# Kernel tuning notes

Measured on AMD Instinct MI355X. Metric: run time of the kernel, lower is better.

The kernel has to match this reference:

```python
import jax, jax.numpy as jnp
import numpy as np
import math

B, S, D, H = 16, 1024, 1024, 16
HD = D // H                      # 64 head dim
MLP_H = int(int(D * 4.0) * 2 / 3)  # 2730 SwiGLU hidden
EPS = 1e-6


def _rmsnorm(h, w):
    # fp32 RMSNorm over last dim
    v = jnp.mean(h * h, axis=-1, keepdims=True)
    return w * (h * jax.lax.rsqrt(v + EPS))


def _rope(x):
    # x: [B, H, S, HD]; standard rotary, half-split convention
    hd = x.shape[-1]
    pos = jnp.arange(x.shape[-2], dtype=jnp.float32)
    inv = 1.0 / (10000.0 ** (jnp.arange(0, hd, 2, dtype=jnp.float32) / hd))
    fr = pos[:, None] * inv[None, :]          # [S, HD/2]
    cos, sin = jnp.cos(fr), jnp.sin(fr)
    x1, x2 = jnp.split(x, 2, axis=-1)
    return jnp.concatenate([x1 * cos - x2 * sin, x1 * sin + x2 * cos], axis=-1)


def setup_inputs() -> dict:
    key = jax.random.key(0)
    ks = jax.random.split(key, 16)
    sc = 0.02
    return {
        "x": jax.random.normal(ks[0], (B, S, D), jnp.float32),
        "c": jax.random.normal(ks[1], (B, D), jnp.float32),
        "w_qkv": jax.random.normal(ks[2], (D, 3 * D), jnp.float32) * sc,
        "b_qkv": jnp.zeros((3 * D,), jnp.float32),
        "w_proj": jax.random.normal(ks[3], (D, D), jnp.float32) * sc,
        "b_proj": jnp.zeros((D,), jnp.float32),
        "w12": jax.random.normal(ks[4], (D, 2 * MLP_H), jnp.float32) * sc,
        "b12": jnp.zeros((2 * MLP_H,), jnp.float32),
        "w3": jax.random.normal(ks[5], (MLP_H, D), jnp.float32) * sc,
        "b3": jnp.zeros((D,), jnp.float32),
        "w_ada": jax.random.normal(ks[6], (D, 6 * D), jnp.float32) * sc,
        "b_ada": jnp.zeros((6 * D,), jnp.float32),
        "norm1_w": jnp.ones((D,), jnp.float32),
        "norm2_w": jnp.ones((D,), jnp.float32),
        "qn_w": jnp.ones((HD,), jnp.float32),
        "kn_w": jnp.ones((HD,), jnp.float32),
    }


def _forward(x, c, w_qkv, b_qkv, w_proj, b_proj, w12, b12, w3, b3,
             w_ada, b_ada, norm1_w, norm2_w, qn_w, kn_w):
    # adaLN modulation params
    ada = jax.nn.silu(c) @ w_ada + b_ada               # [B, 6D]
    sh_a, sc_a, g_a, sh_m, sc_m, g_m = jnp.split(ada, 6, axis=-1)

    def modulate(h, shift, scale):
        return h * (1.0 + scale[:, None, :]) + shift[:, None, :]

    # --- attention branch ---
    h = modulate(_rmsnorm(x, norm1_w), sh_a, sc_a)     # [B, S, D]
    qkv = (h @ w_qkv + b_qkv).reshape(B, S, 3, H, HD)
    qkv = jnp.transpose(qkv, (2, 0, 3, 1, 4))          # [3, B, H, S, HD]
    q, k, v = qkv[0], qkv[1], qkv[2]
    q = _rope(_rmsnorm(q, qn_w))
    k = _rope(_rmsnorm(k, kn_w))
    scores = jnp.einsum('bhqd,bhkd->bhqk', q, k) / math.sqrt(HD)
    attn = jax.nn.softmax(scores, axis=-1)
    o = jnp.einsum('bhqk,bhkd->bhqd', attn, v)         # [B, H, S, HD]
    o = jnp.transpose(o, (0, 2, 1, 3)).reshape(B, S, D)
    o = o @ w_proj + b_proj
    x = x + g_a[:, None, :] * o

    # --- SwiGLU MLP branch ---
    h = modulate(_rmsnorm(x, norm2_w), sh_m, sc_m)
    x12 = h @ w12 + b12
    x1, x2 = jnp.split(x12, 2, axis=-1)
    mlp = (jax.nn.silu(x1) * x2) @ w3 + b3
    return x + g_m[:, None, :] * mlp


def reference(x, c, w_qkv, b_qkv, w_proj, b_proj, w12, b12, w3, b3,
              w_ada, b_ada, norm1_w, norm2_w, qn_w, kn_w):
    return _forward(x, c, w_qkv, b_qkv, w_proj, b_proj, w12, b12, w3, b3,
                    w_ada, b_ada, norm1_w, norm2_w, qn_w, kn_w)
```

## Files before the change

kernel.cpp:

```cpp
#include <hip/hip_runtime.h>
#include <hip/hip_bf16.h>
#include <math.h>

namespace {

constexpr int Bb = 16;
constexpr int Ss = 1024;
constexpr int Dd = 1024;
constexpr int Hh = 16;
constexpr int HD = 64;
constexpr int MLPH = 2730;
constexpr int MLPH_PAD = 2752;
constexpr int ADA_LD = 6144;
constexpr int NR = Bb * Ss;

typedef __attribute__((ext_vector_type(8))) short bf16x8;
typedef __attribute__((ext_vector_type(4))) float f32x4;
typedef __hip_bfloat16 bf16;
typedef unsigned int u32;

__device__ __forceinline__ float bf2f(bf16 v){ return __bfloat162float(v); }
__device__ __forceinline__ bf16 f2bf(float v){ return __float2bfloat16(v); }
__device__ __forceinline__ short f2bfs(float v){ bf16 t = __float2bfloat16(v); return __builtin_bit_cast(short, t); }

__device__ __forceinline__ f32x4 mfma16(bf16x8 a, bf16x8 b, f32x4 c){
  return __builtin_amdgcn_mfma_f32_16x16x32_bf16(a, b, c, 0, 0, 0);
}

__device__ __forceinline__ void gload16(const void* g, void* l){
  __builtin_amdgcn_global_load_lds(
      (const __attribute__((address_space(1))) u32*)g,
      (__attribute__((address_space(3))) u32*)l, 16, 0, 0);
}


__global__ void k_silu(const float* __restrict__ c, float* __restrict__ out, int n){
  int i = blockIdx.x*256 + threadIdx.x;
  if(i < n){ float v = c[i]; out[i] = v / (1.f + __expf(-v)); }
}

__global__ __launch_bounds__(256) void k_ada(const float* __restrict__ sc,
    const float* __restrict__ w, const float* __restrict__ bias, float* __restrict__ ada){
  __shared__ float red[4][Bb][64];
  int tid = threadIdx.x;
  int jj = tid & 63, ks = tid >> 6;
  int j = blockIdx.x*64 + jj;
  float acc[Bb];
  #pragma unroll
  for(int b=0;b<Bb;++b) acc[b] = 0.f;
  for(int k=ks*256; k<ks*256+256; ++k){
    float wv = w[(size_t)k*ADA_LD + j];
    #pragma unroll
    for(int b=0;b<Bb;++b) acc[b] += sc[b*Dd + k] * wv;
  }
  #pragma unroll
  for(int b=0;b<Bb;++b) red[ks][b][jj] = acc[b];
  __syncthreads();
  #pragma unroll
  for(int rep=0;rep<4;++rep){
    int idx = rep*256 + tid;
    int b = idx >> 6, j2 = idx & 63;
    float s = red[0][b][j2]+red[1][b][j2]+red[2][b][j2]+red[3][b][j2];
    ada[(size_t)b*ADA_LD + blockIdx.x*64 + j2] = s + bias[blockIdx.x*64 + j2];
  }
}

__global__ void k_rope_tab(float2* __restrict__ tab){
  int i = blockIdx.x*256 + threadIdx.x;
  int s = i >> 5, f = i & 31;
  float inv = powf(10000.f, -((float)(2*f)) / 64.f);
  float fr = (float)s * inv;
  float sv, cv;
  sincosf(fr, &sv, &cv);
  tab[i] = make_float2(cv, sv);
}

__global__ void k_transpose(const float* __restrict__ in, bf16* __restrict__ out,
                            int R, int C, int Rpad){
  __shared__ short tile[32][33];
  int tx = threadIdx.x & 31, ty = threadIdx.x >> 5;
  int tr0 = blockIdx.x*32, tc0 = blockIdx.y*32;
  #pragma unroll
  for(int i=0;i<4;++i){
    int r = tr0 + ty + i*8, cc = tc0 + tx;
    short v = 0;
    if(r < R && cc < C) v = f2bfs(in[(size_t)r*C + cc]);
    tile[ty+i*8][tx] = v;
  }
  __syncthreads();
  #pragma unroll
  for(int i=0;i<4;++i){
    int oc = tc0 + ty + i*8;
    int orow = tr0 + tx;
    if(oc < C && orow < Rpad)
      out[(size_t)oc*Rpad + orow] = __builtin_bit_cast(bf16, tile[tx][ty+i*8]);
  }
}

__global__ __launch_bounds__(256) void k_norm_mod(const float* __restrict__ x,
    const float* __restrict__ w, const float* __restrict__ shift, const float* __restrict__ scale,
    bf16* __restrict__ out){
  int r = blockIdx.x;
  int b = r >> 10;
  int t = threadIdx.x;
  const float* xr = x + (size_t)r*Dd;
  float v[4]; float ss = 0.f;
  #pragma unroll
  for(int i=0;i<4;++i){
    float f = xr[t*4+i];
    v[i] = f; ss += f*f;
  }
  #pragma unroll
  for(int m=1;m<64;m<<=1) ss += __shfl_xor(ss, m);
  __shared__ float red[4];
  if((t & 63) == 0) red[t>>6] = ss;
  __syncthreads();
  float tot = red[0]+red[1]+red[2]+red[3];
  float rms = rsqrtf(tot * (1.f/Dd) + 1e-6f);
  #pragma unroll
  for(int i=0;i<4;++i){
    int ccol = t*4+i;
    float h = v[i]*rms*w[ccol];
    float scv = scale[(size_t)b*ADA_LD + ccol];
    float shv = shift[(size_t)b*ADA_LD + ccol];
    out[(size_t)r*Dd + ccol] = f2bf(h*(1.f+scv) + shv);
  }
}

__global__ __launch_bounds__(256) void k_qknorm(bf16* __restrict__ qkv,
    const float* __restrict__ qw, const float* __restrict__ kw, const float2* __restrict__ tab){
  int gid = blockIdx.x*256 + threadIdx.x;
  int lane = gid & 63;
  int wid = gid >> 6;
  int isK = wid & 1;
  int bsh = wid >> 1;
  int h = bsh & (Hh-1);
  int bs = bsh >> 4;
  int s = bs & (Ss-1);
  bf16* p = qkv + (size_t)bs*3072 + isK*Dd + h*HD + lane;
  float vv = bf2f(*p);
  float ss = vv*vv;
  #pragma unroll
  for(int m=1;m<64;m<<=1) ss += __shfl_xor(ss, m);
  float rms = rsqrtf(ss*(1.f/HD) + 1e-6f);
  const float* wn = isK ? kw : qw;
  float xn = vv*rms*wn[lane];
  float other = __shfl_xor(xn, 32);
  float2 cs = tab[s*32 + (lane & 31)];
  float o = (lane < 32) ? (xn*cs.x - other*cs.y) : (other*cs.y + xn*cs.x);
  *p = f2bf(o);
}

template<int MODE>
__global__ __launch_bounds__(256, 2) void k_gemm(
    const bf16* __restrict__ A, int lda,
    const bf16* __restrict__ BT, long long b2off, int ldb,
    const float* __restrict__ bias1, const float* __restrict__ bias2,
    int K,
    const float* __restrict__ res, const float* __restrict__ gate,
    void* __restrict__ outp, int ldo)
{
  constexpr int BN  = (MODE==3) ? 64 : 128;
  constexpr int NFR = (MODE==3) ? 2  : 4;
  alignas(16) __shared__ short As[2][128*32];
  alignas(16) __shared__ short Bs[2][BN*32];
  alignas(16) __shared__ short Bs2[(MODE==3)?2:1][(MODE==3)?BN*32:8];

  int tid = threadIdx.x;
  int lane = tid & 63, wid = tid >> 6;
  int wm = wid >> 1, wn = wid & 1;
  int l15 = lane & 15, l4 = lane >> 4;
  int brow = blockIdx.x * 128;
  int bcol = blockIdx.y * BN;

  int r0 = tid >> 2, s0 = tid & 3;
  int r1 = r0 + 64;
  int k80 = s0 ^ ((r0 >> 1) & 3);
  int k81 = s0 ^ ((r1 >> 1) & 3);

  const bf16* a0 = A  + (size_t)(brow+r0)*lda + k80*8;
  const bf16* a1 = A  + (size_t)(brow+r1)*lda + k81*8;
  const bf16* b0 = BT + (size_t)(bcol+r0)*ldb + k80*8;
  const bf16* b1 = BT + (size_t)(bcol+r1)*ldb + k81*8;

  f32x4 zero4 = {0.f,0.f,0.f,0.f};
  f32x4 acc[4][NFR], acc2[4][NFR];
  #pragma unroll
  for(int m=0;m<4;++m)
    #pragma unroll
    for(int n=0;n<NFR;++n){ acc[m][n]=zero4; acc2[m][n]=zero4; }

  auto STAGE = [&](int kt, int buf){
    int ko = kt << 5;
    gload16(a0 + ko, &As[buf][tid*8]);
    gload16(a1 + ko, &As[buf][(tid+256)*8]);
    gload16(b0 + ko, &Bs[buf][tid*8]);
    if constexpr (MODE!=3) gload16(b1 + ko, &Bs[buf][(tid+256)*8]);
    if constexpr (MODE==3) gload16(b0 + b2off + ko, &Bs2[buf][tid*8]);
  };

  const int nk = K >> 5;
  STAGE(0, 0);
  __syncthreads();

  int cur = 0;
  for(int kt=0; kt<nk; ++kt){
    if(kt+1 < nk) STAGE(kt+1, cur^1);

    bf16x8 af[4], bfr[NFR], bfr2[NFR];
    #pragma unroll
    for(int m=0;m<4;++m){
      int rr = wm*64 + m*16 + l15;
      int sl = l4 ^ ((rr >> 1) & 3);
      af[m] = *(const bf16x8*)&As[cur][rr*32 + sl*8];
    }
    #pragma unroll
    for(int n=0;n<NFR;++n){
      int rr = wn*(16*NFR) + n*16 + l15;
      int sl = l4 ^ ((rr >> 1) & 3);
      bfr[n] = *(const bf16x8*)&Bs[cur][rr*32 + sl*8];
      if constexpr (MODE==3)
        bfr2[n] = *(const bf16x8*)&Bs2[cur][rr*32 + sl*8];
    }
    #pragma unroll
    for(int m=0;m<4;++m){
      #pragma unroll
      for(int n=0;n<NFR;++n){
        acc[m][n] = mfma16(af[m], bfr[n], acc[m][n]);
        if constexpr (MODE==3) acc2[m][n] = mfma16(af[m], bfr2[n], acc2[m][n]);
      }
    }
    __syncthreads();
    cur ^= 1;
  }

  #pragma unroll
  for(int m=0;m<4;++m){
    #pragma unroll
    for(int n=0;n<NFR;++n){
      #pragma unroll
      for(int j=0;j<4;++j){
        int r  = brow + wm*64 + m*16 + l4*4 + j;
        int cc = bcol + wn*(16*NFR) + n*16 + l15;
        float v = acc[m][n][j];
        if constexpr (MODE==0){
          v += bias1[cc];
          ((bf16*)outp)[(size_t)r*ldo + cc] = f2bf(v);
        } else if constexpr (MODE==1){
          v += bias1[cc];
          int b = r >> 10;
          float xr = res[(size_t)r*Dd + cc];
          ((float*)outp)[(size_t)r*ldo + cc] = xr + gate[(size_t)b*ADA_LD + cc]*v;
        } else {
          float o = 0.f;
          if(cc < MLPH){
            float v1 = v + bias1[cc];
            float v2 = acc2[m][n][j] + bias2[cc];
            o = (v1/(1.f+__expf(-v1)))*v2;
          }
          ((bf16*)outp)[(size_t)r*ldo + cc] = f2bf(o);
        }
      }
    }
  }
}

__global__ __launch_bounds__(256) void k_attn(const bf16* __restrict__ qkv, bf16* __restrict__ obuf){
  alignas(16) __shared__ short Ks[64*64];
  alignas(16) __shared__ short VTs[64*64];
  alignas(16) __shared__ short Ps[128*64];

  int flatb = blockIdx.x;
  int low3 = flatb & 7;
  int rest = flatb >> 3;
  int qb   = rest & 7;
  int bh   = ((rest >> 3) << 3) | low3;
  int b = bh >> 4, h = bh & 15;

  int tid = threadIdx.x;
  int lane = tid & 63, w = tid >> 6;
  int l15 = lane & 15, l4 = lane >> 4;

  const bf16* base = qkv + (size_t)b*Ss*3072 + h*HD;

  bf16x8 aq[2][2];
  #pragma unroll
  for(int hi=0;hi<2;++hi)
    #pragma unroll
    for(int hf=0;hf<2;++hf)
      aq[hi][hf] = *(const bf16x8*)(base +
          (size_t)(qb*128 + w*32 + hi*16 + l15)*3072 + hf*32 + l4*8);

  int r0 = tid >> 3, c0 = tid & 7;
  int khcol = (c0 ^ (r0 & 7)) * 8;
  bf16x8 kreg[2], vreg[2];
  #pragma unroll
  for(int ch=0; ch<2; ++ch){
    int rr = r0 + ch*32;
    kreg[ch] = *(const bf16x8*)(base + Dd   + (size_t)rr*3072 + khcol);
    vreg[ch] = *(const bf16x8*)(base + 2*Dd + (size_t)rr*3072 + c0*8);
  }

  f32x4 zero4 = {0.f,0.f,0.f,0.f};
  f32x4 acc_o[2][4];
  float mrow[2][4], lrow[2][4];
  #pragma unroll
  for(int hi=0;hi<2;++hi)
    #pragma unroll
    for(int j=0;j<4;++j){ mrow[hi][j] = -1e30f; lrow[hi][j] = 0.f; acc_o[hi][j] = zero4; }

  const float SC = 0.125f * 1.44269504089f;

  for(int kb=0; kb<Ss/64; ++kb){
    if(kb) __syncthreads();
    #pragma unroll
    for(int ch=0; ch<2; ++ch){
      *(bf16x8*)&Ks[(tid + ch*256)*8] = kreg[ch];
      int vr = r0 + ch*32;
      #pragma unroll
      for(int i=0;i<8;++i){
        int g = i ^ c0;
        VTs[(c0*8 + i)*64 + (vr ^ (g<<3))] = vreg[ch][i];
      }
    }
    if(kb+1 < Ss/64){
      #pragma unroll
      for(int ch=0; ch<2; ++ch){
        int rr = (kb+1)*64 + r0 + ch*32;
        kreg[ch] = *(const bf16x8*)(base + Dd   + (size_t)rr*3072 + khcol);
        vreg[ch] = *(const bf16x8*)(base + 2*Dd + (size_t)rr*3072 + c0*8);
      }
    }
    __syncthreads();

    #pragma unroll
    for(int hi=0; hi<2; ++hi){
      f32x4 sacc[4];
      #pragma unroll
      for(int an=0;an<4;++an) sacc[an]=zero4;
      __builtin_amdgcn_s_setprio(1);
      #pragma unroll
      for(int an=0;an<4;++an){
        int R = an*16 + l15;
        bf16x8 bk0 = *(const bf16x8*)&Ks[R*64 + ((l4     ^ (R&7)))*8];
        bf16x8 bk1 = *(const bf16x8*)&Ks[R*64 + (((4|l4) ^ (R&7)))*8];
        sacc[an] = mfma16(aq[hi][0], bk0, sacc[an]);
        sacc[an] = mfma16(aq[hi][1], bk1, sacc[an]);
      }
      __builtin_amdgcn_s_setprio(0);
      #pragma unroll
      for(int j=0;j<4;++j){
        float mx = -1e30f;
        #pragma unroll
        for(int an=0;an<4;++an){ sacc[an][j] *= SC; mx = fmaxf(mx, sacc[an][j]); }
        #pragma unroll
        for(int msk=1;msk<16;msk<<=1) mx = fmaxf(mx, __shfl_xor(mx, msk));
        float mnew = fmaxf(mrow[hi][j], mx);
        float corr = exp2f(mrow[hi][j] - mnew);
        mrow[hi][j] = mnew;
        float psum = 0.f;
        #pragma unroll
        for(int an=0;an<4;++an){
          float p = exp2f(sacc[an][j] - mnew);
          sacc[an][j] = p; psum += p;
        }
        #pragma unroll
        for(int msk=1;msk<16;msk<<=1) psum += __shfl_xor(psum, msk);
        lrow[hi][j] = lrow[hi][j]*corr + psum;
        #pragma unroll
        for(int an=0;an<4;++an) acc_o[hi][an][j] *= corr;
      }
      #pragma unroll
      for(int an=0;an<4;++an)
        #pragma unroll
        for(int j=0;j<4;++j){
          int prw = w*32 + hi*16 + l4*4 + j;
          Ps[prw*64 + ((an*16 + l15) ^ ((prw & 7) << 3))] = f2bfs(sacc[an][j]);
        }
      int prow = w*32 + hi*16 + l15;
      int pg = (l15 & 7) << 3;
      bf16x8 pa0 = *(const bf16x8*)&Ps[prow*64 + ((l4*8)      ^ pg)];
      bf16x8 pa1 = *(const bf16x8*)&Ps[prow*64 + ((32 + l4*8) ^ pg)];
      __builtin_amdgcn_s_setprio(1);
      #pragma unroll
      for(int an2=0;an2<4;++an2){
        int dR = an2*16 + l15;
        int g = ((dR & 7) ^ ((dR >> 3) & 7)) << 3;
        bf16x8 bv0 = *(const bf16x8*)&VTs[dR*64 + ((l4*8)      ^ g)];
        bf16x8 bv1 = *(const bf16x8*)&VTs[dR*64 + ((32 + l4*8) ^ g)];
        acc_o[hi][an2] = mfma16(pa0, bv0, acc_o[hi][an2]);
        acc_o[hi][an2] = mfma16(pa1, bv1, acc_o[hi][an2]);
      }
      __builtin_amdgcn_s_setprio(0);
    }
  }
  #pragma unroll
  for(int hi=0;hi<2;++hi)
    #pragma unroll
    for(int an2=0;an2<4;++an2)
      #pragma unroll
      for(int j=0;j<4;++j){
        int r = qb*128 + w*32 + hi*16 + l4*4 + j;
        float ov = acc_o[hi][an2][j] / lrow[hi][j];
        obuf[((size_t)b*Ss + r)*Dd + h*HD + an2*16 + l15] = f2bf(ov);
      }
}

}

extern "C" void kernel_launch(void* const* d_in, const int* in_sizes, int n_in,
                              void* d_out, int out_size, void* d_ws, size_t ws_size,
                              hipStream_t stream){
  const float* x      = (const float*)d_in[0];
  const float* c      = (const float*)d_in[1];
  const float* w_qkv  = (const float*)d_in[2];
  const float* b_qkv  = (const float*)d_in[3];
  const float* w_proj = (const float*)d_in[4];
  const float* b_proj = (const float*)d_in[5];
  const float* w12    = (const float*)d_in[6];
  const float* b12    = (const float*)d_in[7];
  const float* w3     = (const float*)d_in[8];
  const float* b3     = (const float*)d_in[9];
  const float* w_ada  = (const float*)d_in[10];
  const float* b_ada  = (const float*)d_in[11];
  const float* n1w    = (const float*)d_in[12];
  const float* n2w    = (const float*)d_in[13];
  const float* qnw    = (const float*)d_in[14];
  const float* knw    = (const float*)d_in[15];
  float* out = (float*)d_out;
  (void)in_sizes; (void)n_in; (void)out_size;

  constexpr size_t WS_NEED = 227254272ull;
  if (ws_size < WS_NEED) return;

  char* ws = (char*)d_ws;
  float*  silu_c = (float*)(ws + 0);
  float*  ada    = (float*)(ws + 65536);
  float2* ropet  = (float2*)(ws + 458752);
  bf16*   wqkvT  = (bf16*)(ws + 720896);
  bf16*   wprojT = (bf16*)(ws + 7012352);
  bf16*   w12T   = (bf16*)(ws + 9109504);
  bf16*   w3T    = (bf16*)(ws + 20291584);
  bf16*   hbuf   = (bf16*)(ws + 25927680);
  bf16*   qkvb   = (bf16*)(ws + 59482112);
  float*  xmid   = (float*)(ws + 160145408);
  bf16*   obuf   = hbuf;
  bf16*   h2     = hbuf;
  bf16*   mlpmid = qkvb;

  k_silu<<<64,256,0,stream>>>(c, silu_c, Bb*Dd);
  k_rope_tab<<<128,256,0,stream>>>(ropet);
  k_ada<<<96,256,0,stream>>>(silu_c, w_ada, b_ada, ada);
  k_transpose<<<dim3(32,96),256,0,stream>>>(w_qkv, wqkvT, 1024, 3072, 1024);
  k_transpose<<<dim3(32,32),256,0,stream>>>(w_proj, wprojT, 1024, 1024, 1024);
  k_transpose<<<dim3(32,171),256,0,stream>>>(w12, w12T, 1024, 5460, 1024);
  k_transpose<<<dim3(86,32),256,0,stream>>>(w3, w3T, 2730, 1024, 2752);

  k_norm_mod<<<NR,256,0,stream>>>(x, n1w, ada + 0, ada + 1024, hbuf);
  k_gemm<0><<<dim3(128,24),256,0,stream>>>(hbuf,1024, wqkvT,0,1024,
      b_qkv,nullptr, 1024, nullptr,nullptr, qkvb,3072);
  k_qknorm<<<131072,256,0,stream>>>(qkvb, qnw, knw, ropet);
  k_attn<<<2048,256,0,stream>>>(qkvb, obuf);
  k_gemm<1><<<dim3(128,8),256,0,stream>>>(obuf,1024, wprojT,0,1024,
      b_proj,nullptr, 1024, x, ada + 2048, xmid,1024);

  k_norm_mod<<<NR,256,0,stream>>>(xmid, n2w, ada + 3072, ada + 4096, h2);
  k_gemm<3><<<dim3(128,43),256,0,stream>>>(h2,1024, w12T,(long long)MLPH*1024,1024,
      b12, b12 + MLPH, 1024, nullptr,nullptr, mlpmid, MLPH_PAD);
  k_gemm<1><<<dim3(128,8),256,0,stream>>>(mlpmid,MLPH_PAD, w3T,0,MLPH_PAD,
      b3,nullptr, MLPH_PAD, xmid, ada + 5120, out,1024);
}
```

Baseline: 1.061 ms.

## Vectorize QK-norm/RoPE, fold softmax scale into Q, and lazily rescale attention

The QK RMSNorm+RoPE kernel now has each thread handle 8 contiguous bf16 values with 16-byte loads and stores, one block per token, and shuffles packed partners instead of one element per thread. The softmax scale and log2e are folded into Q at that stage. The attention kernel swaps the MFMA operand order so each lane holds one query row, which cuts the per-row shuffle reductions. It also adds a threshold-based lazy rescale, so the running max and accumulator correction are updated only when any lane's max grows by more than a margin. This trims exp, shuffle and rescale work in the inner loop, but the lazy update and folding the scale before bf16 rounding slightly change numerics and risk overflow headroom.

```diff
diff --git a/kernel.cpp b/kernel.cpp
--- a/kernel.cpp
+++ b/kernel.cpp
@@ -128,27 +128,51 @@
 }
 
 __global__ __launch_bounds__(256) void k_qknorm(bf16* __restrict__ qkv,
-    const float* __restrict__ qw, const float* __restrict__ kw, const float2* __restrict__ tab){
-  int gid = blockIdx.x*256 + threadIdx.x;
-  int lane = gid & 63;
-  int wid = gid >> 6;
-  int isK = wid & 1;
-  int bsh = wid >> 1;
-  int h = bsh & (Hh-1);
-  int bs = bsh >> 4;
+    const float* __restrict__ qw, const float* __restrict__ kw,
+    const float2* __restrict__ tab){
+  int bs = blockIdx.x;
   int s = bs & (Ss-1);
-  bf16* p = qkv + (size_t)bs*3072 + isK*Dd + h*HD + lane;
-  float vv = bf2f(*p);
-  float ss = vv*vv;
-  #pragma unroll
-  for(int m=1;m<64;m<<=1) ss += __shfl_xor(ss, m);
+  int tid = threadIdx.x;
+  int wv = tid >> 6, lane = tid & 63;
+  int isK = wv >> 1;
+  int chunk = (wv & 1)*64 + lane;
+  int c = chunk & 7;
+  int h = chunk >> 3;
+  int dih = c*8;
+  bf16* p = qkv + (size_t)bs*3072 + isK*Dd + h*HD + dih;
+  bf16x8 v = *(const bf16x8*)p;
+  float x[8]; float ss = 0.f;
+  #pragma unroll
+  for(int i=0;i<8;++i){ x[i] = bf2f(__builtin_bit_cast(bf16,(short)v[i])); ss += x[i]*x[i]; }
+  ss += __shfl_xor(ss,1); ss += __shfl_xor(ss,2); ss += __shfl_xor(ss,4);
   float rms = rsqrtf(ss*(1.f/HD) + 1e-6f);
   const float* wn = isK ? kw : qw;
-  float xn = vv*rms*wn[lane];
-  float other = __shfl_xor(xn, 32);
-  float2 cs = tab[s*32 + (lane & 31)];
-  float o = (lane < 32) ? (xn*cs.x - other*cs.y) : (other*cs.y + xn*cs.x);
-  *p = f2bf(o);
+  float xn[8];
+  #pragma unroll
+  for(int i=0;i<8;++i) xn[i] = x[i]*rms*wn[dih+i];
+  u32 pk[4], pq[4];
+  #pragma unroll
+  for(int i=0;i<4;++i)
+    pk[i] = (u32)(unsigned short)f2bfs(xn[2*i]) |
+            ((u32)(unsigned short)f2bfs(xn[2*i+1]) << 16);
+  #pragma unroll
+  for(int i=0;i<4;++i) pq[i] = __shfl_xor((int)pk[i], 4);
+  float px[8];
+  #pragma unroll
+  for(int i=0;i<4;++i){
+    px[2*i]   = bf2f(__builtin_bit_cast(bf16,(short)(pq[i] & 0xffff)));
+    px[2*i+1] = bf2f(__builtin_bit_cast(bf16,(short)(pq[i] >> 16)));
+  }
+  const float2* tb = tab + s*32 + (c & 3)*8;
+  float qs = isK ? 1.f : 0.18033688f;
+  bf16x8 o;
+  #pragma unroll
+  for(int i=0;i<8;++i){
+    float2 cs = tb[i];
+    float r = (c < 4) ? (xn[i]*cs.x - px[i]*cs.y) : (px[i]*cs.y + xn[i]*cs.x);
+    o[i] = f2bfs(r*qs);
+  }
+  *(bf16x8*)p = o;
 }
 
 template<int MODE>
@@ -303,13 +327,15 @@
 
   f32x4 zero4 = {0.f,0.f,0.f,0.f};
   f32x4 acc_o[2][4];
-  float mrow[2][4], lrow[2][4];
-  #pragma unroll
-  for(int hi=0;hi<2;++hi)
-    #pragma unroll
-    for(int j=0;j<4;++j){ mrow[hi][j] = -1e30f; lrow[hi][j] = 0.f; acc_o[hi][j] = zero4; }
-
-  const float SC = 0.125f * 1.44269504089f;
+  float mrow[2], lrow[2];
+  #pragma unroll
+  for(int hi=0;hi<2;++hi){
+    mrow[hi] = -1e30f; lrow[hi] = 0.f;
+    #pragma unroll
+    for(int an=0;an<4;++an) acc_o[hi][an] = zero4;
+  }
+
+  const float THR = 11.54f;
 
   for(int kb=0; kb<Ss/64; ++kb){
     if(kb) __syncthreads();
@@ -344,41 +370,51 @@
         int R = an*16 + l15;
         bf16x8 bk0 = *(const bf16x8*)&Ks[R*64 + ((l4     ^ (R&7)))*8];
         bf16x8 bk1 = *(const bf16x8*)&Ks[R*64 + (((4|l4) ^ (R&7)))*8];
-        sacc[an] = mfma16(aq[hi][0], bk0, sacc[an]);
-        sacc[an] = mfma16(aq[hi][1], bk1, sacc[an]);
+        sacc[an] = mfma16(bk0, aq[hi][0], sacc[an]);
+        sacc[an] = mfma16(bk1, aq[hi][1], sacc[an]);
       }
       __builtin_amdgcn_s_setprio(0);
-      #pragma unroll
-      for(int j=0;j<4;++j){
-        float mx = -1e30f;
+
+      float mx = -1e30f;
+      #pragma unroll
+      for(int an=0;an<4;++an)
         #pragma unroll
-        for(int an=0;an<4;++an){ sacc[an][j] *= SC; mx = fmaxf(mx, sacc[an][j]); }
+        for(int j=0;j<4;++j) mx = fmaxf(mx, sacc[an][j]);
+      mx = fmaxf(mx, __shfl_xor(mx, 16));
+      mx = fmaxf(mx, __shfl_xor(mx, 32));
+      bool grow = mx > mrow[hi] + THR;
+      if(__any(grow)){
+        float mnew = fmaxf(mrow[hi], mx);
+        float corr = exp2f(mrow[hi] - mnew);
+        mrow[hi] = mnew;
+        lrow[hi] *= corr;
+        float cj[4];
         #pragma unroll
-        for(int msk=1;msk<16;msk<<=1) mx = fmaxf(mx, __shfl_xor(mx, msk));
-        float mnew = fmaxf(mrow[hi][j], mx);
-        float corr = exp2f(mrow[hi][j] - mnew);
-        mrow[hi][j] = mnew;
-        float psum = 0.f;
+        for(int j=0;j<4;++j) cj[j] = __shfl(corr, l4*4 + j);
         #pragma unroll
-        for(int an=0;an<4;++an){
-          float p = exp2f(sacc[an][j] - mnew);
-          sacc[an][j] = p; psum += p;
-        }
-        #pragma unroll
-        for(int msk=1;msk<16;msk<<=1) psum += __shfl_xor(psum, msk);
-        lrow[hi][j] = lrow[hi][j]*corr + psum;
-        #pragma unroll
-        for(int an=0;an<4;++an) acc_o[hi][an][j] *= corr;
-      }
+        for(int an=0;an<4;++an)
+          #pragma unroll
+          for(int j=0;j<4;++j) acc_o[hi][an][j] *= cj[j];
+      }
+      float psum = 0.f;
       #pragma unroll
       for(int an=0;an<4;++an)
         #pragma unroll
         for(int j=0;j<4;++j){
-          int prw = w*32 + hi*16 + l4*4 + j;
-          Ps[prw*64 + ((an*16 + l15) ^ ((prw & 7) << 3))] = f2bfs(sacc[an][j]);
+          float pv = exp2f(sacc[an][j] - mrow[hi]);
+          sacc[an][j] = pv; psum += pv;
         }
+      psum += __shfl_xor(psum, 16);
+      psum += __shfl_xor(psum, 32);
+      lrow[hi] += psum;
+
       int prow = w*32 + hi*16 + l15;
       int pg = (l15 & 7) << 3;
+      #pragma unroll
+      for(int an=0;an<4;++an)
+        #pragma unroll
+        for(int j=0;j<4;++j)
+          Ps[prow*64 + ((an*16 + l4*4 + j) ^ pg)] = f2bfs(sacc[an][j]);
       bf16x8 pa0 = *(const bf16x8*)&Ps[prow*64 + ((l4*8)      ^ pg)];
       bf16x8 pa1 = *(const bf16x8*)&Ps[prow*64 + ((32 + l4*8) ^ pg)];
       __builtin_amdgcn_s_setprio(1);
@@ -395,15 +431,19 @@
     }
   }
   #pragma unroll
-  for(int hi=0;hi<2;++hi)
+  for(int hi=0;hi<2;++hi){
+    float lr[4];
+    #pragma unroll
+    for(int j=0;j<4;++j) lr[j] = __shfl(lrow[hi], l4*4 + j);
     #pragma unroll
     for(int an2=0;an2<4;++an2)
       #pragma unroll
       for(int j=0;j<4;++j){
         int r = qb*128 + w*32 + hi*16 + l4*4 + j;
-        float ov = acc_o[hi][an2][j] / lrow[hi][j];
+        float ov = acc_o[hi][an2][j] / lr[j];
         obuf[((size_t)b*Ss + r)*Dd + h*HD + an2*16 + l15] = f2bf(ov);
       }
+  }
 }
 
 }
@@ -459,7 +499,7 @@
   k_norm_mod<<<NR,256,0,stream>>>(x, n1w, ada + 0, ada + 1024, hbuf);
   k_gemm<0><<<dim3(128,24),256,0,stream>>>(hbuf,1024, wqkvT,0,1024,
       b_qkv,nullptr, 1024, nullptr,nullptr, qkvb,3072);
-  k_qknorm<<<131072,256,0,stream>>>(qkvb, qnw, knw, ropet);
+  k_qknorm<<<NR,256,0,stream>>>(qkvb, qnw, knw, ropet);
   k_attn<<<2048,256,0,stream>>>(qkvb, obuf);
   k_gemm<1><<<dim3(128,8),256,0,stream>>>(obuf,1024, wprojT,0,1024,
       b_proj,nullptr, 1024, x, ada + 2048, xmid,1024);
```

After: 937.7 us. 11.6% less time.
